# Performance work log

Measured on AMD Instinct MI355X. Metric: run time of the kernel, lower is better.

## Reference

```python
import jax, jax.numpy as jnp
import numpy as np

D, N, K = 6, 32768, 16          # depths, nodes per depth, max children
V, DIN, DOUT = 100000, 64, 64   # vocab, embed dim, hidden dim


def setup_inputs() -> dict:
    key = jax.random.key(0)
    ks = jax.random.split(key, 6)
    labels = jax.random.randint(ks[0], (D, N), 0, V, dtype=jnp.int32)
    # child index 0 == no child (masked); 1..N index previous depth's nodes
    child_idx = jax.random.randint(ks[1], (D, N, K), 0, N + 1, dtype=jnp.int32)
    E = jax.random.uniform(ks[2], (V, DIN), jnp.float32, -0.05, 0.05)
    s_in = 1.0 / np.sqrt(DIN)
    W_w = jax.random.uniform(ks[3], (DIN, 4 * DOUT), jnp.float32, -s_in, s_in)
    W_b = jnp.zeros((4 * DOUT,), jnp.float32)
    s_out = 1.0 / np.sqrt(DOUT)
    U_f = jax.random.uniform(ks[4], (DOUT, DOUT), jnp.float32, -s_out, s_out)
    U_iuo = jax.random.uniform(ks[5], (DOUT, 3 * DOUT), jnp.float32, -s_out, s_out)
    return {"labels": labels, "child_idx": child_idx, "E": E,
            "W_w": W_w, "W_b": W_b, "U_f": U_f, "U_iuo": U_iuo}


def _tree_lstm(labels, child_idx, E, W_w, W_b, U_f, U_iuo):
    d = U_f.shape[0]
    n = labels.shape[1]
    zero_row = jnp.zeros((1, d), jnp.float32)

    def step(carry, inp):
        h_prev, c_prev = carry            # [N+1, d], row 0 = zero init state
        lab, idx = inp                    # [N], [N, K]
        x = E[lab]                        # [N, din] embedding lookup
        mask = (idx != 0).astype(jnp.float32)   # [N, K]
        h = h_prev[idx]                   # [N, K, d] gather children hidden
        c = c_prev[idx]                   # [N, K, d] gather children cell
        h_sum = jnp.einsum('nkd,nk->nd', h, mask)  # masked child-sum
        Wx = x @ W_w + W_b                # [N, 4d]
        W_f_x, W_i_x, W_u_x, W_o_x = jnp.split(Wx, 4, axis=-1)
        # per-child forget gate
        f_k = jax.nn.sigmoid(W_f_x[:, None, :] + jnp.einsum('nkd,de->nke', h, U_f))
        branch_f = jnp.einsum('nkd,nkd,nk->nd', f_k, c, mask)
        iuo = h_sum @ U_iuo               # [N, 3d]
        i_g = jax.nn.sigmoid(iuo[:, :d] + W_i_x)
        u_g = jnp.tanh(iuo[:, d:2 * d] + W_u_x)
        o_g = jax.nn.sigmoid(iuo[:, 2 * d:] + W_o_x)
        new_c = i_g * u_g + branch_f
        new_h = o_g * jnp.tanh(new_c)
        h_next = jnp.concatenate([zero_row, new_h], 0)
        c_next = jnp.concatenate([zero_row, new_c], 0)
        return (h_next, c_next), None

    init = (jnp.zeros((n + 1, d), jnp.float32), jnp.zeros((n + 1, d), jnp.float32))
    (h_fin, _c_fin), _ = jax.lax.scan(step, init, (labels, child_idx))
    return h_fin[1:]                      # final-depth (roots) hidden [N, d]


def reference(labels, child_idx, E, W_w, W_b, U_f, U_iuo):
    return _tree_lstm(labels, child_idx, E, W_w, W_b, U_f, U_iuo)
```

## Files before the change

kernel.cpp:

```cpp
#include <hip/hip_runtime.h>

#define NN 32768
#define KK 16
#define DD 6

typedef short short8 __attribute__((ext_vector_type(8)));
typedef float floatx4 __attribute__((ext_vector_type(4)));

__device__ __forceinline__ float sigm(float x) { return 1.0f / (1.0f + __expf(-x)); }
__device__ __forceinline__ float ftanh(float x) {
    float e = __expf(2.0f * x);
    return 1.0f - 2.0f / (e + 1.0f);
}
__device__ __forceinline__ unsigned short f2bf(float x) {
    union { float f; unsigned u; } v; v.f = x;
    unsigned r = v.u + 0x7FFF + ((v.u >> 16) & 1);
    return (unsigned short)(r >> 16);
}
__device__ __forceinline__ float bf2f(unsigned short h) {
    union { unsigned u; float f; } v; v.u = ((unsigned)h) << 16; return v.f;
}

__global__ __launch_bounds__(256) void k0_all(
    const int* __restrict__ labels, const float* __restrict__ E,
    const float* __restrict__ W_w, const float* __restrict__ W_b,
    float* __restrict__ WxAll)
{
    __shared__ int labs[64];
    __shared__ __align__(16) unsigned short Ax[64][72];
    __shared__ __align__(16) unsigned short Bw[256][72];
    const int tid = threadIdx.x;
    const int blk = blockIdx.x & 511;
    const int dep = blockIdx.x >> 9;
    const int n0 = blk * 64;
    float* __restrict__ Wx = WxAll + (size_t)dep * NN * 256;
    if (tid < 64) labs[tid] = labels[(size_t)dep * NN + n0 + tid];
    __syncthreads();
    {
        const int m = tid >> 2, q = tid & 3;
        const float4* e4 = (const float4*)(E + (size_t)labs[m] * 64 + q * 16);
#pragma unroll
        for (int i = 0; i < 4; ++i) {
            float4 v = e4[i];
            Ax[m][q * 16 + i * 4 + 0] = f2bf(v.x);
            Ax[m][q * 16 + i * 4 + 1] = f2bf(v.y);
            Ax[m][q * 16 + i * 4 + 2] = f2bf(v.z);
            Ax[m][q * 16 + i * 4 + 3] = f2bf(v.w);
        }
    }
    {
        const int c = tid;
#pragma unroll 4
        for (int k = 0; k < 64; ++k) Bw[c][k] = f2bf(W_w[k * 256 + c]);
    }
    __syncthreads();
    const int ln = tid & 63, wv = tid >> 6;
    const int lr = ln & 15, qd = ln >> 4;
    short8 af[2];
#pragma unroll
    for (int ks = 0; ks < 2; ++ks)
        af[ks] = *(const short8*)&Ax[wv * 16 + lr][ks * 32 + qd * 8];
    floatx4 acc[16];
#pragma unroll
    for (int nt = 0; nt < 16; ++nt) acc[nt] = (floatx4){0.f, 0.f, 0.f, 0.f};
#pragma unroll
    for (int nt = 0; nt < 16; ++nt) {
#pragma unroll
        for (int ks = 0; ks < 2; ++ks) {
            short8 bw = *(const short8*)&Bw[nt * 16 + lr][ks * 32 + qd * 8];
            acc[nt] = __builtin_amdgcn_mfma_f32_16x16x32_bf16(af[ks], bw, acc[nt], 0, 0, 0);
        }
    }
#pragma unroll
    for (int nt = 0; nt < 16; ++nt) {
        const int col = nt * 16 + lr;
        const float bb = W_b[col];
#pragma unroll
        for (int r = 0; r < 4; ++r) {
            const int node = n0 + wv * 16 + qd * 4 + r;
            Wx[(size_t)node * 256 + col] = acc[nt][r] + bb;
        }
    }
}

__global__ __launch_bounds__(256) void kd_fused(
    const int* __restrict__ cidx, const float* __restrict__ sprev,
    const float* __restrict__ Wx, const float* __restrict__ U_iuo,
    const float* __restrict__ U_f, float* __restrict__ snext,
    float* __restrict__ out, int first, int last)
{
    __shared__ __align__(16) unsigned short Bi[192][72];
    __shared__ __align__(16) unsigned short Bf[64][72];
    __shared__ __align__(16) unsigned short Ah[64][72];
    __shared__ __align__(16) unsigned short AlHs[64][72];
    const int tid = threadIdx.x;
    const int n0 = blockIdx.x * 64;
    if (tid < 192) {
        const int c = tid;
#pragma unroll 4
        for (int k = 0; k < 64; ++k) Bi[c][k] = f2bf(U_iuo[k * 192 + c]);
    } else {
        const int c = tid - 192;
#pragma unroll 4
        for (int k = 0; k < 64; ++k) Bf[c][k] = f2bf(U_f[k * 64 + c]);
    }
    const int ln = tid & 63, wv = tid >> 6;
    const int lr = ln & 15, qd = ln >> 4;

    float hs[4][4] = {{0.f}}, bfv[4][4] = {{0.f}};
    if (!first) {
        float wfx[4][4];
#pragma unroll
        for (int r = 0; r < 4; ++r)
#pragma unroll
            for (int nt = 0; nt < 4; ++nt)
                wfx[r][nt] = Wx[(size_t)(n0 + wv * 16 + qd * 4 + r) * 256 + nt * 16 + lr];
        const unsigned* __restrict__ su = (const unsigned*)sprev;
        const _Float16* __restrict__ chh = (const _Float16*)sprev;
        for (int k = 0; k < KK; ++k) {
            int id[4];
#pragma unroll
            for (int r = 0; r < 4; ++r)
                id[r] = cidx[(size_t)(n0 + wv * 16 + qd * 4 + r) * KK + k];
            unsigned hg[4][4];
            float cc[4][4];
#pragma unroll
            for (int r = 0; r < 4; ++r)
#pragma unroll
                for (int nt = 0; nt < 4; ++nt)
                    hg[r][nt] = su[(size_t)id[r] * 96 + nt * 16 + lr];
#pragma unroll
            for (int r = 0; r < 4; ++r)
#pragma unroll
                for (int nt = 0; nt < 4; ++nt)
                    cc[r][nt] = (float)chh[(size_t)id[r] * 192 + 128 + nt * 16 + lr];
#pragma unroll
            for (int r = 0; r < 4; ++r)
#pragma unroll
                for (int nt = 0; nt < 4; ++nt) {
                    const float h = (float)(short)(hg[r][nt] & 0xFFFFu) * (1.f / 32767.f);
                    const float g = (float)((int)hg[r][nt] >> 16) * (1.f / 2048.f);
                    hs[r][nt] += h;
                    bfv[r][nt] = fmaf(sigm(wfx[r][nt] + g), cc[r][nt], bfv[r][nt]);
                }
        }
    }
#pragma unroll
    for (int r = 0; r < 4; ++r)
#pragma unroll
        for (int nt = 0; nt < 4; ++nt) {
            const int m = wv * 16 + qd * 4 + r, col = nt * 16 + lr;
            const unsigned short hi = f2bf(hs[r][nt]);
            Ah[m][col] = hi;
            AlHs[m][col] = f2bf(hs[r][nt] - bf2f(hi));
        }
    __syncthreads();

    short8 ah[2], al[2];
#pragma unroll
    for (int ks = 0; ks < 2; ++ks) {
        ah[ks] = *(const short8*)&Ah[wv * 16 + lr][ks * 32 + qd * 8];
        al[ks] = *(const short8*)&AlHs[wv * 16 + lr][ks * 32 + qd * 8];
    }
    floatx4 ai[4], au[4], ao[4];
#pragma unroll
    for (int nt = 0; nt < 4; ++nt) {
        ai[nt] = (floatx4){0.f, 0.f, 0.f, 0.f};
        au[nt] = (floatx4){0.f, 0.f, 0.f, 0.f};
        ao[nt] = (floatx4){0.f, 0.f, 0.f, 0.f};
    }
#pragma unroll
    for (int nt = 0; nt < 4; ++nt) {
#pragma unroll
        for (int ks = 0; ks < 2; ++ks) {
            short8 b0 = *(const short8*)&Bi[nt * 16 + lr][ks * 32 + qd * 8];
            short8 b1 = *(const short8*)&Bi[64 + nt * 16 + lr][ks * 32 + qd * 8];
            short8 b2 = *(const short8*)&Bi[128 + nt * 16 + lr][ks * 32 + qd * 8];
            ai[nt] = __builtin_amdgcn_mfma_f32_16x16x32_bf16(al[ks], b0, ai[nt], 0, 0, 0);
            ai[nt] = __builtin_amdgcn_mfma_f32_16x16x32_bf16(ah[ks], b0, ai[nt], 0, 0, 0);
            au[nt] = __builtin_amdgcn_mfma_f32_16x16x32_bf16(al[ks], b1, au[nt], 0, 0, 0);
            au[nt] = __builtin_amdgcn_mfma_f32_16x16x32_bf16(ah[ks], b1, au[nt], 0, 0, 0);
            ao[nt] = __builtin_amdgcn_mfma_f32_16x16x32_bf16(al[ks], b2, ao[nt], 0, 0, 0);
            ao[nt] = __builtin_amdgcn_mfma_f32_16x16x32_bf16(ah[ks], b2, ao[nt], 0, 0, 0);
        }
    }
    float nhv[4][4];
#pragma unroll
    for (int nt = 0; nt < 4; ++nt) {
        const int col = nt * 16 + lr;
#pragma unroll
        for (int r = 0; r < 4; ++r) {
            const int node = n0 + wv * 16 + qd * 4 + r;
            const float* __restrict__ wxr = Wx + (size_t)node * 256;
            const float ig = sigm(ai[nt][r] + wxr[64 + col]);
            const float ug = ftanh(au[nt][r] + wxr[128 + col]);
            const float og = sigm(ao[nt][r] + wxr[192 + col]);
            const float nc = fmaf(ig, ug, bfv[r][nt]);
            const float nh = og * ftanh(nc);
            nhv[nt][r] = nh;
            if (last) {
                out[(size_t)node * 64 + col] = nh;
            } else {
                ((_Float16*)snext)[(size_t)(node + 1) * 192 + 128 + col] = (_Float16)nc;
                AlHs[wv * 16 + qd * 4 + r][col] = f2bf(nh);
            }
        }
    }
    if (!last) {
        short8 ag[2];
#pragma unroll
        for (int ks = 0; ks < 2; ++ks)
            ag[ks] = *(const short8*)&AlHs[wv * 16 + lr][ks * 32 + qd * 8];
        floatx4 g[4];
#pragma unroll
        for (int nt = 0; nt < 4; ++nt) g[nt] = (floatx4){0.f, 0.f, 0.f, 0.f};
#pragma unroll
        for (int nt = 0; nt < 4; ++nt) {
#pragma unroll
            for (int ks = 0; ks < 2; ++ks) {
                short8 bfr = *(const short8*)&Bf[nt * 16 + lr][ks * 32 + qd * 8];
                g[nt] = __builtin_amdgcn_mfma_f32_16x16x32_bf16(ag[ks], bfr, g[nt], 0, 0, 0);
            }
        }
        unsigned* __restrict__ su = (unsigned*)snext;
#pragma unroll
        for (int nt = 0; nt < 4; ++nt) {
#pragma unroll
            for (int r = 0; r < 4; ++r) {
                const int node = n0 + wv * 16 + qd * 4 + r;
                const int hq = (int)rintf(nhv[nt][r] * 32767.f);
                const int gq = (int)rintf(g[nt][r] * 2048.f);
                su[(size_t)(node + 1) * 96 + nt * 16 + lr] =
                    ((unsigned)hq & 0xFFFFu) | ((unsigned)gq << 16);
            }
        }
        if (blockIdx.x == 0 && tid < 96)
            ((unsigned*)snext)[tid] = 0u;
    }
}

extern "C" void kernel_launch(void* const* d_in, const int* in_sizes, int n_in,
                              void* d_out, int out_size, void* d_ws, size_t ws_size,
                              hipStream_t stream)
{
    const int*   labels = (const int*)d_in[0];
    const int*   child  = (const int*)d_in[1];
    const float* E      = (const float*)d_in[2];
    const float* W_w    = (const float*)d_in[3];
    const float* W_b    = (const float*)d_in[4];
    const float* U_f    = (const float*)d_in[5];
    const float* U_iuo  = (const float*)d_in[6];
    float* out = (float*)d_out;
    float* ws  = (float*)d_ws;

    const size_t R = (size_t)(NN + 1) * 96;
    float* s0    = ws;
    float* s1    = ws + R;
    float* WxAll = ws + 2 * R;

    k0_all<<<6 * (NN / 64), 256, 0, stream>>>(labels, E, W_w, W_b, WxAll);

    float* sp = s0;
    float* sn = s1;
    for (int d = 0; d < DD; ++d) {
        const int last = (d == DD - 1);
        kd_fused<<<NN / 64, 256, 0, stream>>>(
            child + (size_t)d * NN * KK, sp, WxAll + (size_t)d * NN * 256,
            U_iuo, U_f, sn, out, d == 0, last);
        float* ts = sp; sp = sn; sn = ts;
    }
}
```

Measured before the change: 371.6 us.

## Pack child state as uint2 with fp32 cell and store Wx in fp16

Interleaves each child's packed (h,g) word with its fp32 cell value into one 8-byte uint2, so the gather loop does a single 64-bit load per child element instead of two separate loads. The Wx precompute buffer is stored as fp16 instead of fp32, halving its write and read traffic. LDS row padding changes from 72 to 74 or 68, and the gate GEMM is restructured into a 12-tile loop with the k loop left unrolled once. Cell precision rises to fp32 while Wx drops to fp16, which adds rounding error on the gate preactivations.

```diff
diff --git a/kernel.cpp b/kernel.cpp
--- a/kernel.cpp
+++ b/kernel.cpp
@@ -24,16 +24,16 @@
 __global__ __launch_bounds__(256) void k0_all(
     const int* __restrict__ labels, const float* __restrict__ E,
     const float* __restrict__ W_w, const float* __restrict__ W_b,
-    float* __restrict__ WxAll)
+    _Float16* __restrict__ WxAll)
 {
     __shared__ int labs[64];
-    __shared__ __align__(16) unsigned short Ax[64][72];
-    __shared__ __align__(16) unsigned short Bw[256][72];
+    __shared__ __align__(16) unsigned short Ax[64][74];
+    __shared__ __align__(16) unsigned short Bw[256][74];
     const int tid = threadIdx.x;
     const int blk = blockIdx.x & 511;
     const int dep = blockIdx.x >> 9;
     const int n0 = blk * 64;
-    float* __restrict__ Wx = WxAll + (size_t)dep * NN * 256;
+    _Float16* __restrict__ Wx = WxAll + (size_t)dep * NN * 256;
     if (tid < 64) labs[tid] = labels[(size_t)dep * NN + n0 + tid];
     __syncthreads();
     {
@@ -78,21 +78,21 @@
 #pragma unroll
         for (int r = 0; r < 4; ++r) {
             const int node = n0 + wv * 16 + qd * 4 + r;
-            Wx[(size_t)node * 256 + col] = acc[nt][r] + bb;
+            Wx[(size_t)node * 256 + col] = (_Float16)(acc[nt][r] + bb);
         }
     }
 }
 
 __global__ __launch_bounds__(256) void kd_fused(
-    const int* __restrict__ cidx, const float* __restrict__ sprev,
-    const float* __restrict__ Wx, const float* __restrict__ U_iuo,
-    const float* __restrict__ U_f, float* __restrict__ snext,
+    const int* __restrict__ cidx, const uint2* __restrict__ sprev,
+    const _Float16* __restrict__ Wx, const float* __restrict__ U_iuo,
+    const float* __restrict__ U_f, uint2* __restrict__ snext,
     float* __restrict__ out, int first, int last)
 {
-    __shared__ __align__(16) unsigned short Bi[192][72];
-    __shared__ __align__(16) unsigned short Bf[64][72];
-    __shared__ __align__(16) unsigned short Ah[64][72];
-    __shared__ __align__(16) unsigned short AlHs[64][72];
+    __shared__ __align__(16) unsigned short Bi[192][68];
+    __shared__ __align__(16) unsigned short Bf[64][68];
+    __shared__ __align__(16) unsigned short Ah[64][68];
+    __shared__ __align__(16) unsigned short AlHs[64][68];
     const int tid = threadIdx.x;
     const int n0 = blockIdx.x * 64;
     if (tid < 192) {
@@ -114,34 +114,29 @@
         for (int r = 0; r < 4; ++r)
 #pragma unroll
             for (int nt = 0; nt < 4; ++nt)
-                wfx[r][nt] = Wx[(size_t)(n0 + wv * 16 + qd * 4 + r) * 256 + nt * 16 + lr];
-        const unsigned* __restrict__ su = (const unsigned*)sprev;
-        const _Float16* __restrict__ chh = (const _Float16*)sprev;
+                wfx[r][nt] = (float)Wx[(size_t)(n0 + wv * 16 + qd * 4 + r) * 256
+                                       + nt * 16 + lr];
+#pragma unroll 1
         for (int k = 0; k < KK; ++k) {
             int id[4];
 #pragma unroll
             for (int r = 0; r < 4; ++r)
                 id[r] = cidx[(size_t)(n0 + wv * 16 + qd * 4 + r) * KK + k];
-            unsigned hg[4][4];
-            float cc[4][4];
+            uint2 v[4][4];
 #pragma unroll
             for (int r = 0; r < 4; ++r)
 #pragma unroll
                 for (int nt = 0; nt < 4; ++nt)
-                    hg[r][nt] = su[(size_t)id[r] * 96 + nt * 16 + lr];
+                    v[r][nt] = sprev[(size_t)id[r] * 64 + nt * 16 + lr];
 #pragma unroll
             for (int r = 0; r < 4; ++r)
 #pragma unroll
-                for (int nt = 0; nt < 4; ++nt)
-                    cc[r][nt] = (float)chh[(size_t)id[r] * 192 + 128 + nt * 16 + lr];
-#pragma unroll
-            for (int r = 0; r < 4; ++r)
-#pragma unroll
                 for (int nt = 0; nt < 4; ++nt) {
-                    const float h = (float)(short)(hg[r][nt] & 0xFFFFu) * (1.f / 32767.f);
-                    const float g = (float)((int)hg[r][nt] >> 16) * (1.f / 2048.f);
+                    const float h = (float)(short)(v[r][nt].x & 0xFFFFu) * (1.f / 32767.f);
+                    const float g = (float)((int)v[r][nt].x >> 16) * (1.f / 2048.f);
+                    const float c = __uint_as_float(v[r][nt].y);
                     hs[r][nt] += h;
-                    bfv[r][nt] = fmaf(sigm(wfx[r][nt] + g), cc[r][nt], bfv[r][nt]);
+                    bfv[r][nt] = fmaf(sigm(wfx[r][nt] + g), c, bfv[r][nt]);
                 }
         }
     }
@@ -155,53 +150,42 @@
             AlHs[m][col] = f2bf(hs[r][nt] - bf2f(hi));
         }
     __syncthreads();
-
     short8 ah[2], al[2];
 #pragma unroll
     for (int ks = 0; ks < 2; ++ks) {
         ah[ks] = *(const short8*)&Ah[wv * 16 + lr][ks * 32 + qd * 8];
         al[ks] = *(const short8*)&AlHs[wv * 16 + lr][ks * 32 + qd * 8];
     }
-    floatx4 ai[4], au[4], ao[4];
-#pragma unroll
-    for (int nt = 0; nt < 4; ++nt) {
-        ai[nt] = (floatx4){0.f, 0.f, 0.f, 0.f};
-        au[nt] = (floatx4){0.f, 0.f, 0.f, 0.f};
-        ao[nt] = (floatx4){0.f, 0.f, 0.f, 0.f};
-    }
-#pragma unroll
-    for (int nt = 0; nt < 4; ++nt) {
+    floatx4 acc[12];
+#pragma unroll
+    for (int nt = 0; nt < 12; ++nt) {
+        floatx4 a = (floatx4){0.f, 0.f, 0.f, 0.f};
 #pragma unroll
         for (int ks = 0; ks < 2; ++ks) {
-            short8 b0 = *(const short8*)&Bi[nt * 16 + lr][ks * 32 + qd * 8];
-            short8 b1 = *(const short8*)&Bi[64 + nt * 16 + lr][ks * 32 + qd * 8];
-            short8 b2 = *(const short8*)&Bi[128 + nt * 16 + lr][ks * 32 + qd * 8];
-            ai[nt] = __builtin_amdgcn_mfma_f32_16x16x32_bf16(al[ks], b0, ai[nt], 0, 0, 0);
-            ai[nt] = __builtin_amdgcn_mfma_f32_16x16x32_bf16(ah[ks], b0, ai[nt], 0, 0, 0);
-            au[nt] = __builtin_amdgcn_mfma_f32_16x16x32_bf16(al[ks], b1, au[nt], 0, 0, 0);
-            au[nt] = __builtin_amdgcn_mfma_f32_16x16x32_bf16(ah[ks], b1, au[nt], 0, 0, 0);
-            ao[nt] = __builtin_amdgcn_mfma_f32_16x16x32_bf16(al[ks], b2, ao[nt], 0, 0, 0);
-            ao[nt] = __builtin_amdgcn_mfma_f32_16x16x32_bf16(ah[ks], b2, ao[nt], 0, 0, 0);
-        }
-    }
-    float nhv[4][4];
+            const short8 bu = *(const short8*)&Bi[nt * 16 + lr][ks * 32 + qd * 8];
+            a = __builtin_amdgcn_mfma_f32_16x16x32_bf16(al[ks], bu, a, 0, 0, 0);
+            a = __builtin_amdgcn_mfma_f32_16x16x32_bf16(ah[ks], bu, a, 0, 0, 0);
+        }
+        acc[nt] = a;
+    }
+    float nhv[4][4], ncv[4][4];
 #pragma unroll
     for (int nt = 0; nt < 4; ++nt) {
         const int col = nt * 16 + lr;
 #pragma unroll
         for (int r = 0; r < 4; ++r) {
             const int node = n0 + wv * 16 + qd * 4 + r;
-            const float* __restrict__ wxr = Wx + (size_t)node * 256;
-            const float ig = sigm(ai[nt][r] + wxr[64 + col]);
-            const float ug = ftanh(au[nt][r] + wxr[128 + col]);
-            const float og = sigm(ao[nt][r] + wxr[192 + col]);
+            const _Float16* __restrict__ wxr = Wx + (size_t)node * 256;
+            const float ig = sigm(acc[nt][r] + (float)wxr[64 + col]);
+            const float ug = ftanh(acc[4 + nt][r] + (float)wxr[128 + col]);
+            const float og = sigm(acc[8 + nt][r] + (float)wxr[192 + col]);
             const float nc = fmaf(ig, ug, bfv[r][nt]);
             const float nh = og * ftanh(nc);
             nhv[nt][r] = nh;
+            ncv[nt][r] = nc;
             if (last) {
                 out[(size_t)node * 64 + col] = nh;
             } else {
-                ((_Float16*)snext)[(size_t)(node + 1) * 192 + 128 + col] = (_Float16)nc;
                 AlHs[wv * 16 + qd * 4 + r][col] = f2bf(nh);
             }
         }
@@ -213,16 +197,14 @@
             ag[ks] = *(const short8*)&AlHs[wv * 16 + lr][ks * 32 + qd * 8];
         floatx4 g[4];
 #pragma unroll
-        for (int nt = 0; nt < 4; ++nt) g[nt] = (floatx4){0.f, 0.f, 0.f, 0.f};
-#pragma unroll
         for (int nt = 0; nt < 4; ++nt) {
+            g[nt] = (floatx4){0.f, 0.f, 0.f, 0.f};
 #pragma unroll
             for (int ks = 0; ks < 2; ++ks) {
-                short8 bfr = *(const short8*)&Bf[nt * 16 + lr][ks * 32 + qd * 8];
+                const short8 bfr = *(const short8*)&Bf[nt * 16 + lr][ks * 32 + qd * 8];
                 g[nt] = __builtin_amdgcn_mfma_f32_16x16x32_bf16(ag[ks], bfr, g[nt], 0, 0, 0);
             }
         }
-        unsigned* __restrict__ su = (unsigned*)snext;
 #pragma unroll
         for (int nt = 0; nt < 4; ++nt) {
 #pragma unroll
@@ -230,12 +212,14 @@
                 const int node = n0 + wv * 16 + qd * 4 + r;
                 const int hq = (int)rintf(nhv[nt][r] * 32767.f);
                 const int gq = (int)rintf(g[nt][r] * 2048.f);
-                su[(size_t)(node + 1) * 96 + nt * 16 + lr] =
-                    ((unsigned)hq & 0xFFFFu) | ((unsigned)gq << 16);
+                uint2 pw;
+                pw.x = ((unsigned)hq & 0xFFFFu) | ((unsigned)gq << 16);
+                pw.y = __float_as_uint(ncv[nt][r]);
+                snext[(size_t)(node + 1) * 64 + nt * 16 + lr] = pw;
             }
         }
-        if (blockIdx.x == 0 && tid < 96)
-            ((unsigned*)snext)[tid] = 0u;
+        if (blockIdx.x == 0 && tid < 64)
+            snext[tid] = make_uint2(0u, 0u);
     }
 }
 
@@ -251,22 +235,20 @@
     const float* U_f    = (const float*)d_in[5];
     const float* U_iuo  = (const float*)d_in[6];
     float* out = (float*)d_out;
-    float* ws  = (float*)d_ws;
-
-    const size_t R = (size_t)(NN + 1) * 96;
-    float* s0    = ws;
-    float* s1    = ws + R;
-    float* WxAll = ws + 2 * R;
+
+    uint2* s0 = (uint2*)d_ws;
+    uint2* s1 = s0 + (size_t)(NN + 1) * 64;
+    _Float16* WxAll = (_Float16*)(s1 + (size_t)(NN + 1) * 64);
 
     k0_all<<<6 * (NN / 64), 256, 0, stream>>>(labels, E, W_w, W_b, WxAll);
 
-    float* sp = s0;
-    float* sn = s1;
+    uint2* sp = s0;
+    uint2* sn = s1;
     for (int d = 0; d < DD; ++d) {
         const int last = (d == DD - 1);
         kd_fused<<<NN / 64, 256, 0, stream>>>(
             child + (size_t)d * NN * KK, sp, WxAll + (size_t)d * NN * 256,
             U_iuo, U_f, sn, out, d == 0, last);
-        float* ts = sp; sp = sn; sn = ts;
-    }
-}
+        uint2* ts = sp; sp = sn; sn = ts;
+    }
+}
```

Result: no change. 366.3 us (-1.4%).
